# Performance work log

Hardware: AMD Instinct MI355X
Metric: run time of the kernel (lower is better)

The kernel has to match this reference:

```python
import jax, jax.numpy as jnp
import numpy as np

ROPE_DIM = 64
ROPE_THETA = 10000.0
SLIDING_WINDOW = 1024
_K_MASK = jnp.finfo(jnp.bfloat16).min


def _pos_embeddings(positions, head_dim, rope_theta):
    # positions: [B, T] -> sin, cos: [B, T, head_dim]
    fraction = jnp.arange(0, head_dim, 2, dtype=jnp.float32) / head_dim
    inv_freq = 1.0 / (rope_theta ** fraction)
    sinusoid = jnp.einsum('BT,k->BTk', positions.astype(jnp.float32), inv_freq,
                          precision=jax.lax.Precision.HIGHEST)
    sin = jnp.sin(sinusoid); cos = jnp.cos(sinusoid)
    return jnp.concatenate([sin, sin], -1), jnp.concatenate([cos, cos], -1)


def _rotate_half(x):
    x1, x2 = x[..., :x.shape[-1] // 2], x[..., x.shape[-1] // 2:]
    return jnp.concatenate([-x2, x1], -1)


def _apply_rope_partial(x, sin, cos, rope_dim):
    x_rope, x_nope = x[..., :rope_dim], x[..., rope_dim:]
    sin = sin[:, :, None, :]; cos = cos[:, :, None, :]
    x_rope = x_rope * cos + _rotate_half(x_rope) * sin
    return jnp.concatenate([x_rope, x_nope], -1).astype(x.dtype)


def setup_inputs() -> dict:
    key = jax.random.key(0)
    ks = jax.random.split(key, 6)
    B, T, D = 2, 2048, 2048
    N, K, H, Hv = 16, 4, 128, 128
    S = 2048  # cache size
    sc = 0.02
    return {
        'x': jax.random.normal(ks[0], (B, T, D), jnp.float32),
        'wq': jax.random.normal(ks[1], (D, N, H), jnp.float32) * sc,
        'wk': jax.random.normal(ks[2], (D, K, H), jnp.float32) * sc,
        'wv': jax.random.normal(ks[3], (D, K, Hv), jnp.float32) * sc,
        'wo': jax.random.normal(ks[4], (N, Hv, D), jnp.float32) * sc,
        'sink_bias': jnp.zeros((N,), jnp.float32),
        'k_cache': jnp.zeros((B, S, K, H), jnp.float32),
        'v_cache': jnp.zeros((B, S, K, Hv), jnp.float32),
        'segment_ids': jnp.ones((B, T), jnp.int32),
        'cur_ind': 0,
        'start_ind': -jnp.ones((B,), jnp.int32),
    }


def reference(x, wq, wk, wv, wo, sink_bias, k_cache, v_cache,
              segment_ids, cur_ind, start_ind):
    B, T, D = x.shape
    N, H = wq.shape[1], wq.shape[2]
    K, Hv = wk.shape[1], wv.shape[2]
    n_rep = N // K
    scaling = H ** -0.5
    cur_ind = jnp.asarray(cur_ind, jnp.int32)

    q = jnp.einsum('BTD,DNH->BTNH', x, wq)
    k = jnp.einsum('BSD,DKH->BSKH', x, wk)
    v = jnp.einsum('BSD,DKV->BSKV', x, wv)

    # left pads / positions from segment ids
    left_pads = jnp.sum(jnp.cumsum(segment_ids != 0, axis=-1) == 0, -1).astype(jnp.int32)
    start = jnp.where(start_ind < 0, left_pads, start_ind)
    pos = jax.vmap(lambda row: jnp.where(row != 0,
                                         jnp.arange(T, dtype=jnp.int32) - jnp.argmax(row).astype(jnp.int32),
                                         2 ** 30))(segment_ids) + cur_ind
    sin, cos = _pos_embeddings(pos, ROPE_DIM, ROPE_THETA)
    q = _apply_rope_partial(q, sin, cos, ROPE_DIM)
    k = _apply_rope_partial(k, sin, cos, ROPE_DIM)

    # KV cache append
    kc = jax.lax.dynamic_update_slice(k_cache, k, (0, cur_ind, 0, 0))
    vc = jax.lax.dynamic_update_slice(v_cache, v, (0, cur_ind, 0, 0))
    S = kc.shape[1]

    # GQA repeat
    kr = jnp.repeat(kc[:, :, :, None, :], n_rep, axis=3).reshape(B, S, N, H)
    vr = jnp.repeat(vc[:, :, :, None, :], n_rep, axis=3).reshape(B, S, N, Hv)

    logits = jnp.einsum('BTNH,BSNH->BTNS', q, kr) * scaling

    q_pos = cur_ind + jnp.arange(T, dtype=jnp.int32)[None, :] - start[:, None]
    ts = jnp.arange(S, dtype=jnp.int32)
    kv_seg = (ts[None, :] >= start[:, None]) & (ts[None, :] < cur_ind + T)
    k_pos = ts[None, :] - start[:, None]
    causal = k_pos[:, None, :] <= q_pos[:, :, None]
    seg_mask = kv_seg[:, None, :] == segment_ids[:, :, None]
    window = k_pos[:, None, :] >= q_pos[:, :, None] - (SLIDING_WINDOW - 1)
    final_mask = causal & seg_mask & window  # [B, T, S]
    logits = jnp.where(final_mask[:, :, None, :], logits, _K_MASK)

    # attention sink bias: extra softmax slot per head
    sink = jnp.broadcast_to(sink_bias[None, None, :, None], (B, T, N, 1))
    logits = jnp.concatenate([logits, sink], axis=-1)
    weights = jax.nn.softmax(logits.astype(jnp.float32), axis=-1).astype(logits.dtype)
    weights = weights[..., :-1]

    attn = jnp.einsum('BTNS,BSNV->BTNV', weights, vr)
    return jnp.einsum('BTNV,NVD->BTD', attn, wo)
```

## Files before the change

### kernel.cpp

```cpp
#include <hip/hip_runtime.h>
#include <hip/hip_bf16.h>
#include <stdint.h>

#define BB 2
#define TT 2048
#define DD 2048
#define NHQ 16
#define KH 4
#define HD 128
#define SS 2048
#define WINDOW 1024
#define M2FIX 12.0f
#define QSC_LOG2E 0.12751751f
#define LOG2E 1.4426950408889634f
#define NLOG2F 0.4152410118609203f

typedef __attribute__((ext_vector_type(8))) short bf16x8;
typedef __attribute__((ext_vector_type(4))) float f32x4;
typedef __attribute__((ext_vector_type(16))) float f32x16;

#define MFMA16(a, b, c) __builtin_amdgcn_mfma_f32_16x16x32_bf16(a, b, c, 0, 0, 0)
#define MFMA32(a, b, c) __builtin_amdgcn_mfma_f32_32x32x16_bf16(a, b, c, 0, 0, 0)

__device__ __forceinline__ ushort f2bf(float f) {
  uint32_t u = __float_as_uint(f);
  u += 0x7FFF + ((u >> 16) & 1);
  return (ushort)(u >> 16);
}
__device__ __forceinline__ ushort f2bf_trunc(float f) {
  return (ushort)(__float_as_uint(f) >> 16);
}
__device__ __forceinline__ float bf2f(ushort h) {
  return __uint_as_float(((uint32_t)h) << 16);
}

__device__ __forceinline__ void async_copy16(const ushort* g, ushort* l) {
  __builtin_amdgcn_global_load_lds(
      (const __attribute__((address_space(1))) uint32_t*)g,
      (__attribute__((address_space(3))) uint32_t*)l, 16, 0, 0);
}

__device__ __forceinline__ void tr_tile(const float* __restrict__ in,
                                        ushort* __restrict__ out,
                                        int C, int ldo, int cx, int cy) {
  __shared__ float tile[32][33];
  int tx = threadIdx.x & 31, ty = threadIdx.x >> 5;
  int r0 = cy * 32, c0 = cx * 32;
#pragma unroll
  for (int k = 0; k < 4; k++)
    tile[ty + k * 8][tx] = in[(size_t)(r0 + ty + k * 8) * C + c0 + tx];
  __syncthreads();
#pragma unroll
  for (int k = 0; k < 4; k++)
    out[(size_t)(c0 + ty + k * 8) * ldo + r0 + tx] = f2bf(tile[tx][ty + k * 8]);
}

__global__ void prep_fused(const float* __restrict__ x, const float* __restrict__ wq,
                           const float* __restrict__ wk, const float* __restrict__ wv,
                           const float* __restrict__ wo, const int* __restrict__ seg,
                           const int* __restrict__ start_ind, ushort* __restrict__ xb,
                           ushort* __restrict__ WcatT, ushort* __restrict__ WoT,
                           int* __restrict__ meta) {
  int bz = blockIdx.x;
  int tid = threadIdx.x;
  if (bz < 2) {
    __shared__ int red[256];
    int b = bz;
    int first = TT;
    for (int t = tid; t < TT; t += 256)
      if (seg[b * TT + t] != 0) first = min(first, t);
    red[tid] = first;
    __syncthreads();
    for (int s = 128; s > 0; s >>= 1) {
      if (tid < s) red[tid] = min(red[tid], red[tid + s]);
      __syncthreads();
    }
    if (tid == 0) {
      int fi = red[0];
      int st = start_ind[b] < 0 ? fi : start_ind[b];
      meta[b * 2 + 0] = st;
      meta[b * 2 + 1] = (fi >= TT) ? 0 : fi;
    }
    return;
  }
  bz -= 2;
  if (bz < 2048) {
#pragma unroll
    for (int p = 0; p < 4; p++) {
      int i = bz * 1024 + p * 256 + tid;
      float4 v = ((const float4*)x)[i];
      ushort4 o;
      o.x = f2bf(v.x); o.y = f2bf(v.y); o.z = f2bf(v.z); o.w = f2bf(v.w);
      ((ushort4*)xb)[i] = o;
    }
    return;
  }
  bz -= 2048;
  if (bz < 4096) { tr_tile(wq, WcatT, 2048, 2048, bz & 63, bz >> 6); return; }
  bz -= 4096;
  if (bz < 1024) { tr_tile(wk, WcatT + (size_t)2048 * 2048, 512, 2048, bz & 15, bz >> 4); return; }
  bz -= 1024;
  if (bz < 1024) { tr_tile(wv, WcatT + (size_t)2560 * 2048, 512, 2048, bz & 15, bz >> 4); return; }
  bz -= 1024;
  tr_tile(wo, WoT, 2048, 2048, bz & 63, bz >> 6);
}

__global__ void transpose_v(const ushort* __restrict__ in, ushort* __restrict__ out) {
  __shared__ ushort tile[32][33];
  int mtx = blockIdx.z;
  in  += (size_t)mtx * SS * HD;
  out += (size_t)mtx * SS * HD;
  int tx = threadIdx.x & 31, ty = threadIdx.x >> 5;
  int s0 = blockIdx.x * 32, h0 = blockIdx.y * 32;
#pragma unroll
  for (int k = 0; k < 4; k++)
    tile[ty + k * 8][tx] = in[(size_t)(s0 + ty + k * 8) * HD + h0 + tx];
  __syncthreads();
#pragma unroll
  for (int k = 0; k < 4; k++) {
    int h = h0 + ty + k * 8;
    int s = s0 + tx;
    int cit = (s & 63) >> 3;
    int sout = (s & ~63) | ((cit ^ (h & 7)) << 3) | (s & 7);
    out[(size_t)h * SS + sout] = tile[tx][ty + k * 8];
  }
}

__global__ __launch_bounds__(256) void gemm_qkv(const ushort* __restrict__ A,
                                                const ushort* __restrict__ Bt,
                                                const int* __restrict__ seg,
                                                const int* __restrict__ cur_p,
                                                const int* __restrict__ meta,
                                                ushort* __restrict__ qa,
                                                ushort* __restrict__ ka,
                                                ushort* __restrict__ va) {
  const int K = DD;
  __shared__ ushort As[128 * 64];
  __shared__ ushort Bs[128 * 64];
  __shared__ float posf_s[128];
  int tid = threadIdx.x;
  int lane = tid & 63, wave = tid >> 6;
  int wr = wave >> 1, wc = wave & 1;
  int row0 = blockIdx.y * 128, col0 = blockIdx.x * 128;
  int l31 = lane & 31, khalf = lane >> 5, lx8 = l31 & 7;
  int cur = cur_p[0];

  if (tid < 128) {
    int m = row0 + tid;
    int bb = m >> 11, t = m & 2047;
    int segv = seg[m];
    int first = meta[bb * 2 + 1];
    posf_s[tid] = (segv != 0) ? (float)(t - first + cur) : 1073741824.0f;
  }

  f32x16 acc[2][2];
#pragma unroll
  for (int i = 0; i < 2; i++)
#pragma unroll
    for (int j = 0; j < 2; j++)
#pragma unroll
      for (int e = 0; e < 16; e++) acc[i][j][e] = 0.f;

  int srow = tid >> 3, scol = tid & 7;
  int ssw = (scol ^ (srow & 7)) * 8;
  const ushort* Ag = A  + (size_t)(row0 + srow) * K + ssw;
  const ushort* Bg = Bt + (size_t)(col0 + srow) * K + ssw;
  ushort* AsD = As + tid * 8;
  ushort* BsD = Bs + tid * 8;

  for (int kc = 0; kc < K; kc += 64) {
    __syncthreads();
#pragma unroll
    for (int p = 0; p < 4; p++)
      async_copy16(Ag + kc + (size_t)(p * 32) * K, AsD + p * 2048);
#pragma unroll
    for (int p = 0; p < 4; p++)
      async_copy16(Bg + kc + (size_t)(p * 32) * K, BsD + p * 2048);
    __syncthreads();
#pragma unroll
    for (int ks = 0; ks < 4; ks++) {
      bf16x8 af[2], bfm[2];
      int ch = (ks * 2 + khalf) ^ lx8;
#pragma unroll
      for (int i = 0; i < 2; i++)
        af[i] = *(const bf16x8*)(As + (wr * 64 + i * 32 + l31) * 64 + ch * 8);
#pragma unroll
      for (int j = 0; j < 2; j++)
        bfm[j] = *(const bf16x8*)(Bs + (wc * 64 + j * 32 + l31) * 64 + ch * 8);
#pragma unroll
      for (int i = 0; i < 2; i++)
#pragma unroll
        for (int j = 0; j < 2; j++)
          acc[i][j] = MFMA32(af[i], bfm[j], acc[i][j]);
    }
  }

  int cb0 = col0 + wc * 64;
  int region = (cb0 < 2048) ? 0 : (cb0 < 2560 ? 1 : 2);
  bool ropehalf = ((cb0 & 64) == 0) && (region <= 1);
  int hbase = cb0 & 64;
  float invf = exp2f(-NLOG2F * (float)l31);

#pragma unroll
  for (int i = 0; i < 2; i++) {
#pragma unroll
    for (int reg = 0; reg < 16; reg++) {
      int rloc = wr * 64 + i * 32 + (reg & 3) + 8 * (reg >> 2) + 4 * khalf;
      int m = row0 + rloc;
      int b = m >> 11, t = m & 2047;
      float v0 = acc[i][0][reg], v1 = acc[i][1][reg];
      if (ropehalf) {
        float posf = posf_s[rloc];
        float sn, cs;
        __sincosf(posf * invf, &sn, &cs);
        float n0 = v0 * cs - v1 * sn;
        v1 = v1 * cs + v0 * sn;
        v0 = n0;
      }
      if (region == 0) {
        int head = cb0 >> 7;
        size_t base = ((size_t)(b * NHQ + head) * TT + t) * HD + hbase;
        qa[base + l31]      = f2bf(v0 * QSC_LOG2E);
        qa[base + 32 + l31] = f2bf(v1 * QSC_LOG2E);
      } else if (region == 1) {
        int head = (cb0 - 2048) >> 7;
        size_t rowbase = ((size_t)(b * KH + head) * SS + t) * HD;
        int sw = t & 7;
        int c0x = hbase + l31, c1x = hbase + 32 + l31;
        ka[rowbase + ((((c0x >> 3) ^ sw) << 3) | (c0x & 7))] = f2bf(v0);
        ka[rowbase + ((((c1x >> 3) ^ sw) << 3) | (c1x & 7))] = f2bf(v1);
      } else {
        int head = (cb0 - 2560) >> 7;
        size_t base = ((size_t)(b * KH + head) * SS + t) * HD + hbase;
        va[base + l31]      = f2bf(v0);
        va[base + 32 + l31] = f2bf(v1);
      }
    }
  }
}

template <int OUT_F32>
__global__ __launch_bounds__(256) void gemm_bt(const ushort* __restrict__ A,
                                               const ushort* __restrict__ Bt,
                                               void* __restrict__ Cout,
                                               int M, int N, int K) {
  __shared__ ushort As[128 * 64];
  __shared__ ushort Bs[128 * 64];
  int tid = threadIdx.x;
  int lane = tid & 63, wave = tid >> 6;
  int wr = wave >> 1, wc = wave & 1;
  int row0 = blockIdx.y * 128, col0 = blockIdx.x * 128;
  int l31 = lane & 31, khalf = lane >> 5, lx8 = l31 & 7;

  f32x16 acc[2][2];
#pragma unroll
  for (int i = 0; i < 2; i++)
#pragma unroll
    for (int j = 0; j < 2; j++)
#pragma unroll
      for (int e = 0; e < 16; e++) acc[i][j][e] = 0.f;

  int srow = tid >> 3, scol = tid & 7;
  int ssw = (scol ^ (srow & 7)) * 8;
  const ushort* Ag = A  + (size_t)(row0 + srow) * K + ssw;
  const ushort* Bg = Bt + (size_t)(col0 + srow) * K + ssw;
  ushort* AsD = As + tid * 8;
  ushort* BsD = Bs + tid * 8;

  for (int kc = 0; kc < K; kc += 64) {
    __syncthreads();
#pragma unroll
    for (int p = 0; p < 4; p++)
      async_copy16(Ag + kc + (size_t)(p * 32) * K, AsD + p * 2048);
#pragma unroll
    for (int p = 0; p < 4; p++)
      async_copy16(Bg + kc + (size_t)(p * 32) * K, BsD + p * 2048);
    __syncthreads();
#pragma unroll
    for (int ks = 0; ks < 4; ks++) {
      bf16x8 af[2], bfm[2];
      int ch = (ks * 2 + khalf) ^ lx8;
#pragma unroll
      for (int i = 0; i < 2; i++)
        af[i] = *(const bf16x8*)(As + (wr * 64 + i * 32 + l31) * 64 + ch * 8);
#pragma unroll
      for (int j = 0; j < 2; j++)
        bfm[j] = *(const bf16x8*)(Bs + (wc * 64 + j * 32 + l31) * 64 + ch * 8);
#pragma unroll
      for (int i = 0; i < 2; i++)
#pragma unroll
        for (int j = 0; j < 2; j++)
          acc[i][j] = MFMA32(af[i], bfm[j], acc[i][j]);
    }
  }

#pragma unroll
  for (int i = 0; i < 2; i++)
#pragma unroll
    for (int reg = 0; reg < 16; reg++) {
      int r = row0 + wr * 64 + i * 32 + (reg & 3) + 8 * (reg >> 2) + 4 * khalf;
#pragma unroll
      for (int j = 0; j < 2; j++) {
        int c = col0 + wc * 64 + j * 32 + l31;
        float v = acc[i][j][reg];
        if (OUT_F32)
          ((float*)Cout)[(size_t)r * N + c] = v;
        else
          ((ushort*)Cout)[(size_t)r * N + c] = f2bf(v);
      }
    }
}

__global__ __launch_bounds__(256) void flash_attn(
    const ushort* __restrict__ qa, const ushort* __restrict__ ka,
    const ushort* __restrict__ vat, const float* __restrict__ sink_bias,
    const int* __restrict__ seg, const int* __restrict__ cur_p,
    const int* __restrict__ meta, ushort* __restrict__ Obuf) {
  __shared__ ushort Ks[64 * 128];
  __shared__ ushort VT[128 * 64];
  __shared__ ushort Ps[4 * 16 * 64];

  int bx = blockIdx.x;
  int u = bx & 255, v = bx >> 8;
  int combo = u & 31, j5 = u >> 5;
  int b = combo >> 4, n = combo & 15;
  int qt = (v == 0) ? j5 : (v == 1) ? (15 - j5) : (v == 2) ? (16 + j5) : (31 - j5);
  int kb = n >> 2;
  int t0 = qt * 64;
  int cur = cur_p[0];
  int start = meta[b * 2];

  int tid = threadIdx.x, lane = tid & 63, w = tid >> 6;
  int lcol = lane & 15, quad = lane >> 4, lx = lcol & 7;
  int t0w = t0 + w * 16;

  const ushort* qbase = qa + (size_t)(b * NHQ + n) * TT * HD;
  const ushort* kbase = ka + (size_t)(b * KH + kb) * SS * HD;
  const ushort* vtb   = vat + (size_t)(b * KH + kb) * HD * SS;

  bf16x8 qf[4];
  {
    const ushort* qrow = qbase + (size_t)(t0w + lcol) * HD + quad * 8;
#pragma unroll
    for (int c = 0; c < 4; c++) qf[c] = *(const bf16x8*)(qrow + c * 32);
  }

  int segq[4], trow[4];
#pragma unroll
  for (int r = 0; r < 4; r++) {
    trow[r] = t0w + quad * 4 + r;
    segq[r] = seg[b * TT + trow[r]];
  }
  int seg1 = __all(segq[0] == 1 && segq[1] == 1 && segq[2] == 1 && segq[3] == 1);

  f32x4 oacc[8], lacc;
#pragma unroll
  for (int ob = 0; ob < 8; ob++) { f32x4 z = {0.f, 0.f, 0.f, 0.f}; oacc[ob] = z; }
  { f32x4 z = {0.f, 0.f, 0.f, 0.f}; lacc = z; }

  bf16x8 ones;
#pragma unroll
  for (int e = 0; e < 8; e++) ones[e] = (short)0x3F80;

  ushort* KsD = Ks + tid * 8;
  ushort* VTD = VT + tid * 8;
  const ushort* KgT = kbase + tid * 8;
  const ushort* VgT = vtb + (size_t)(tid >> 3) * SS + (tid & 7) * 8;

  int lo = cur + t0 - (WINDOW - 1); if (lo < 0) lo = 0;
  int hi = cur + t0 + 63;           if (hi > SS - 1) hi = SS - 1;
  int ktlo = lo >> 6, kthi = hi >> 6;

  ushort* PsW = Ps + w * 1024;

  for (int kt = ktlo; kt <= kthi; kt++) {
    int ks0 = kt * 64;
    __syncthreads();
#pragma unroll
    for (int p = 0; p < 4; p++)
      async_copy16(KgT + (size_t)ks0 * 128 + p * 2048, KsD + p * 2048);
#pragma unroll
    for (int p = 0; p < 4; p++)
      async_copy16(VgT + ks0 + (size_t)p * 32 * SS, VTD + p * 2048);
    __syncthreads();

    bool active = (ks0 <= cur + t0w + 15) && (ks0 + 63 >= cur + t0w - (WINDOW - 1));
    if (active) {
      f32x4 sacc[4];
#pragma unroll
      for (int cb = 0; cb < 4; cb++) { f32x4 z = {0.f, 0.f, 0.f, 0.f}; sacc[cb] = z; }
#pragma unroll
      for (int c = 0; c < 4; c++) {
#pragma unroll
        for (int cb = 0; cb < 4; cb++) {
          bf16x8 kf = *(const bf16x8*)(Ks + (cb * 16 + lcol) * 128 +
                                       (((c * 4 + quad) ^ lx)) * 8);
          sacc[cb] = MFMA16(qf[c], kf, sacc[cb]);
        }
      }

      bool fast = seg1 && (ks0 >= start) && (ks0 + 63 <= cur + t0w) &&
                  (ks0 >= cur + t0w + 15 - (WINDOW - 1));
      if (fast) {
#pragma unroll
        for (int r = 0; r < 4; r++) {
          int row = quad * 4 + r;
#pragma unroll
          for (int cb = 0; cb < 4; cb++) {
            float p = exp2f(sacc[cb][r] - M2FIX);
            PsW[row * 64 + (((cb * 2 + (lcol >> 3)) ^ (row & 7)) * 8) + lx] = f2bf_trunc(p);
          }
        }
      } else {
        int sidx[4], kvseg[4];
#pragma unroll
        for (int cb = 0; cb < 4; cb++) {
          sidx[cb] = ks0 + cb * 16 + lcol;
          kvseg[cb] = (sidx[cb] >= start && sidx[cb] < cur + TT) ? 1 : 0;
        }
#pragma unroll
        for (int r = 0; r < 4; r++) {
          int row = quad * 4 + r;
          int qp = (segq[r] != 0) ? (cur + trow[r]) : (1 << 29);
#pragma unroll
          for (int cb = 0; cb < 4; cb++) {
            bool ok = (sidx[cb] <= qp) && (sidx[cb] >= qp - (WINDOW - 1)) &&
                      (kvseg[cb] == segq[r]);
            float p = ok ? exp2f(sacc[cb][r] - M2FIX) : 0.f;
            PsW[row * 64 + (((cb * 2 + (lcol >> 3)) ^ (row & 7)) * 8) + lx] = f2bf_trunc(p);
          }
        }
      }

#pragma unroll
      for (int c2 = 0; c2 < 2; c2++) {
        bf16x8 pf = *(const bf16x8*)(PsW + lcol * 64 + (((c2 * 4 + quad) ^ lx)) * 8);
#pragma unroll
        for (int ob = 0; ob < 8; ob++) {
          bf16x8 vf = *(const bf16x8*)(VT + (ob * 16 + lcol) * 64 +
                                       (((c2 * 4 + quad) ^ lx)) * 8);
          oacc[ob] = MFMA16(pf, vf, oacc[ob]);
        }
        lacc = MFMA16(pf, ones, lacc);
      }
    }
  }

  float sb = sink_bias[n];
#pragma unroll
  for (int r = 0; r < 4; r++) {
    float l = lacc[r] + exp2f(sb * LOG2E - M2FIX);
    float inv = 1.f / l;
    int t = trow[r];
    size_t base = ((size_t)(b * TT + t)) * (NHQ * HD) + n * HD;
#pragma unroll
    for (int ob = 0; ob < 8; ob++)
      Obuf[base + ob * 16 + lcol] = f2bf(oacc[ob][r] * inv);
  }
}

extern "C" void kernel_launch(void* const* d_in, const int* in_sizes, int n_in,
                              void* d_out, int out_size, void* d_ws, size_t ws_size,
                              hipStream_t stream) {
  const float* x  = (const float*)d_in[0];
  const float* wq = (const float*)d_in[1];
  const float* wk = (const float*)d_in[2];
  const float* wv = (const float*)d_in[3];
  const float* wo = (const float*)d_in[4];
  const float* sink = (const float*)d_in[5];
  const int* seg = (const int*)d_in[8];
  const int* cur = (const int*)d_in[9];
  const int* start_ind = (const int*)d_in[10];

  char* ws = (char*)d_ws;
  ushort* xb    = (ushort*)(ws + 0);
  ushort* WcatT = (ushort*)(ws + 16777216);
  ushort* WoT   = (ushort*)(ws + 29360128);
  ushort* qa    = (ushort*)(ws + 37748736);
  ushort* ka    = (ushort*)(ws + 54525952);
  ushort* va    = (ushort*)(ws + 58720256);
  ushort* vat   = (ushort*)(ws + 62914560);
  ushort* Obuf  = (ushort*)(ws + 67108864);
  int*    meta  = (int*)(ws + 83886080);

  prep_fused<<<12290, 256, 0, stream>>>(x, wq, wk, wv, wo, seg, start_ind,
                                        xb, WcatT, WoT, meta);
  gemm_qkv<<<dim3(24, 32), 256, 0, stream>>>(xb, WcatT, seg, cur, meta, qa, ka, va);
  transpose_v<<<dim3(64, 4, 8), 256, 0, stream>>>(va, vat);
  flash_attn<<<1024, 256, 0, stream>>>(qa, ka, vat, sink, seg, cur, meta, Obuf);
  gemm_bt<1><<<dim3(16, 32), 256, 0, stream>>>(Obuf, WoT, d_out, 4096, 2048, 2048);
}
```

Before: 296.6 us.

## Enlarge transpose and attention tiles, add extra LDS swizzle bits in GEMMs

The weight transpose-and-convert now works on 64x64 tiles instead of 32x32, which cuts the prep grid from 12290 to 4610 blocks. Flash attention now runs 512-thread blocks over 128-query tiles with 8 waves, so each K/V tile loaded into LDS is shared by twice as many query rows, and the query-tile order is interleaved for load balance. Both GEMMs XOR extra row bits into the LDS swizzle to reduce bank conflicts on the 32-row MFMA fragment reads. Risks are lower occupancy from larger blocks and LDS, and coarser work units in attention.

Measured after the change: 313.7 us. 1.06x slower.

```diff
diff --git a/kernel.cpp b/kernel.cpp
--- a/kernel.cpp
+++ b/kernel.cpp
@@ -40,19 +40,23 @@
       (__attribute__((address_space(3))) uint32_t*)l, 16, 0, 0);
 }
 
-__device__ __forceinline__ void tr_tile(const float* __restrict__ in,
-                                        ushort* __restrict__ out,
-                                        int C, int ldo, int cx, int cy) {
-  __shared__ float tile[32][33];
-  int tx = threadIdx.x & 31, ty = threadIdx.x >> 5;
-  int r0 = cy * 32, c0 = cx * 32;
-#pragma unroll
-  for (int k = 0; k < 4; k++)
-    tile[ty + k * 8][tx] = in[(size_t)(r0 + ty + k * 8) * C + c0 + tx];
+__device__ __forceinline__ void tr_tile64(const float* __restrict__ in,
+                                          ushort* __restrict__ out,
+                                          int C, int ldo, int cx, int cy) {
+  __shared__ float tile[64][65];
+  int tx = threadIdx.x & 63, ty = threadIdx.x >> 6;
+  int r0 = cy * 64, c0 = cx * 64;
+#pragma unroll
+  for (int k = 0; k < 16; k++) {
+    int row = k * 4 + ty;
+    tile[row][tx] = in[(size_t)(r0 + row) * C + c0 + tx];
+  }
   __syncthreads();
 #pragma unroll
-  for (int k = 0; k < 4; k++)
-    out[(size_t)(c0 + ty + k * 8) * ldo + r0 + tx] = f2bf(tile[tx][ty + k * 8]);
+  for (int k = 0; k < 16; k++) {
+    int c = k * 4 + ty;
+    out[(size_t)(c0 + c) * ldo + r0 + tx] = f2bf(tile[tx][c]);
+  }
 }
 
 __global__ void prep_fused(const float* __restrict__ x, const float* __restrict__ wq,
@@ -96,13 +100,13 @@
     return;
   }
   bz -= 2048;
-  if (bz < 4096) { tr_tile(wq, WcatT, 2048, 2048, bz & 63, bz >> 6); return; }
-  bz -= 4096;
-  if (bz < 1024) { tr_tile(wk, WcatT + (size_t)2048 * 2048, 512, 2048, bz & 15, bz >> 4); return; }
+  if (bz < 1024) { tr_tile64(wq, WcatT, 2048, 2048, bz & 31, bz >> 5); return; }
   bz -= 1024;
-  if (bz < 1024) { tr_tile(wv, WcatT + (size_t)2560 * 2048, 512, 2048, bz & 15, bz >> 4); return; }
-  bz -= 1024;
-  tr_tile(wo, WoT, 2048, 2048, bz & 63, bz >> 6);
+  if (bz < 256)  { tr_tile64(wk, WcatT + (size_t)2048 * 2048, 512, 2048, bz & 7, bz >> 3); return; }
+  bz -= 256;
+  if (bz < 256)  { tr_tile64(wv, WcatT + (size_t)2560 * 2048, 512, 2048, bz & 7, bz >> 3); return; }
+  bz -= 256;
+  tr_tile64(wo, WoT, 2048, 2048, bz & 31, bz >> 5);
 }
 
 __global__ void transpose_v(const ushort* __restrict__ in, ushort* __restrict__ out) {
@@ -143,6 +147,7 @@
   int wr = wave >> 1, wc = wave & 1;
   int row0 = blockIdx.y * 128, col0 = blockIdx.x * 128;
   int l31 = lane & 31, khalf = lane >> 5, lx8 = l31 & 7;
+  int rsw = lx8 ^ ((l31 >> 3) & 3);
   int cur = cur_p[0];
 
   if (tid < 128) {
@@ -162,7 +167,7 @@
       for (int e = 0; e < 16; e++) acc[i][j][e] = 0.f;
 
   int srow = tid >> 3, scol = tid & 7;
-  int ssw = (scol ^ (srow & 7)) * 8;
+  int ssw = (scol ^ (srow & 7) ^ ((srow >> 3) & 3)) * 8;
   const ushort* Ag = A  + (size_t)(row0 + srow) * K + ssw;
   const ushort* Bg = Bt + (size_t)(col0 + srow) * K + ssw;
   ushort* AsD = As + tid * 8;
@@ -180,7 +185,7 @@
 #pragma unroll
     for (int ks = 0; ks < 4; ks++) {
       bf16x8 af[2], bfm[2];
-      int ch = (ks * 2 + khalf) ^ lx8;
+      int ch = (ks * 2 + khalf) ^ rsw;
 #pragma unroll
       for (int i = 0; i < 2; i++)
         af[i] = *(const bf16x8*)(As + (wr * 64 + i * 32 + l31) * 64 + ch * 8);
@@ -251,6 +256,7 @@
   int wr = wave >> 1, wc = wave & 1;
   int row0 = blockIdx.y * 128, col0 = blockIdx.x * 128;
   int l31 = lane & 31, khalf = lane >> 5, lx8 = l31 & 7;
+  int rsw = lx8 ^ ((l31 >> 3) & 3);
 
   f32x16 acc[2][2];
 #pragma unroll
@@ -261,7 +267,7 @@
       for (int e = 0; e < 16; e++) acc[i][j][e] = 0.f;
 
   int srow = tid >> 3, scol = tid & 7;
-  int ssw = (scol ^ (srow & 7)) * 8;
+  int ssw = (scol ^ (srow & 7) ^ ((srow >> 3) & 3)) * 8;
   const ushort* Ag = A  + (size_t)(row0 + srow) * K + ssw;
   const ushort* Bg = Bt + (size_t)(col0 + srow) * K + ssw;
   ushort* AsD = As + tid * 8;
@@ -279,7 +285,7 @@
 #pragma unroll
     for (int ks = 0; ks < 4; ks++) {
       bf16x8 af[2], bfm[2];
-      int ch = (ks * 2 + khalf) ^ lx8;
+      int ch = (ks * 2 + khalf) ^ rsw;
 #pragma unroll
       for (int i = 0; i < 2; i++)
         af[i] = *(const bf16x8*)(As + (wr * 64 + i * 32 + l31) * 64 + ch * 8);
@@ -311,22 +317,22 @@
     }
 }
 
-__global__ __launch_bounds__(256) void flash_attn(
+__global__ __launch_bounds__(512) void flash_attn(
     const ushort* __restrict__ qa, const ushort* __restrict__ ka,
     const ushort* __restrict__ vat, const float* __restrict__ sink_bias,
     const int* __restrict__ seg, const int* __restrict__ cur_p,
     const int* __restrict__ meta, ushort* __restrict__ Obuf) {
   __shared__ ushort Ks[64 * 128];
   __shared__ ushort VT[128 * 64];
-  __shared__ ushort Ps[4 * 16 * 64];
+  __shared__ ushort Ps[8 * 16 * 64];
 
   int bx = blockIdx.x;
-  int u = bx & 255, v = bx >> 8;
-  int combo = u & 31, j5 = u >> 5;
-  int b = combo >> 4, n = combo & 15;
-  int qt = (v == 0) ? j5 : (v == 1) ? (15 - j5) : (v == 2) ? (16 + j5) : (31 - j5);
+  int b = bx & 1;
+  int n = (bx >> 1) & 15;
+  int g = bx >> 5;
+  int qp = (g & 1) ? (15 - (g >> 1)) : (g >> 1);
   int kb = n >> 2;
-  int t0 = qt * 64;
+  int t0 = qp * 128;
   int cur = cur_p[0];
   int start = meta[b * 2];
 
@@ -368,7 +374,7 @@
   const ushort* VgT = vtb + (size_t)(tid >> 3) * SS + (tid & 7) * 8;
 
   int lo = cur + t0 - (WINDOW - 1); if (lo < 0) lo = 0;
-  int hi = cur + t0 + 63;           if (hi > SS - 1) hi = SS - 1;
+  int hi = cur + t0 + 127;          if (hi > SS - 1) hi = SS - 1;
   int ktlo = lo >> 6, kthi = hi >> 6;
 
   ushort* PsW = Ps + w * 1024;
@@ -377,11 +383,11 @@
     int ks0 = kt * 64;
     __syncthreads();
 #pragma unroll
-    for (int p = 0; p < 4; p++)
-      async_copy16(KgT + (size_t)ks0 * 128 + p * 2048, KsD + p * 2048);
-#pragma unroll
-    for (int p = 0; p < 4; p++)
-      async_copy16(VgT + ks0 + (size_t)p * 32 * SS, VTD + p * 2048);
+    for (int p = 0; p < 2; p++)
+      async_copy16(KgT + (size_t)ks0 * 128 + p * 4096, KsD + p * 4096);
+#pragma unroll
+    for (int p = 0; p < 2; p++)
+      async_copy16(VgT + ks0 + (size_t)(p * 64) * SS, VTD + p * 4096);
     __syncthreads();
 
     bool active = (ks0 <= cur + t0w + 15) && (ks0 + 63 >= cur + t0w - (WINDOW - 1));
@@ -421,10 +427,10 @@
 #pragma unroll
         for (int r = 0; r < 4; r++) {
           int row = quad * 4 + r;
-          int qp = (segq[r] != 0) ? (cur + trow[r]) : (1 << 29);
+          int qp2 = (segq[r] != 0) ? (cur + trow[r]) : (1 << 29);
 #pragma unroll
           for (int cb = 0; cb < 4; cb++) {
-            bool ok = (sidx[cb] <= qp) && (sidx[cb] >= qp - (WINDOW - 1)) &&
+            bool ok = (sidx[cb] <= qp2) && (sidx[cb] >= qp2 - (WINDOW - 1)) &&
                       (kvseg[cb] == segq[r]);
             float p = ok ? exp2f(sacc[cb][r] - M2FIX) : 0.f;
             PsW[row * 64 + (((cb * 2 + (lcol >> 3)) ^ (row & 7)) * 8) + lx] = f2bf_trunc(p);
@@ -483,10 +489,10 @@
   ushort* Obuf  = (ushort*)(ws + 67108864);
   int*    meta  = (int*)(ws + 83886080);
 
-  prep_fused<<<12290, 256, 0, stream>>>(x, wq, wk, wv, wo, seg, start_ind,
-                                        xb, WcatT, WoT, meta);
+  prep_fused<<<4610, 256, 0, stream>>>(x, wq, wk, wv, wo, seg, start_ind,
+                                       xb, WcatT, WoT, meta);
   gemm_qkv<<<dim3(24, 32), 256, 0, stream>>>(xb, WcatT, seg, cur, meta, qa, ka, va);
   transpose_v<<<dim3(64, 4, 8), 256, 0, stream>>>(va, vat);
-  flash_attn<<<1024, 256, 0, stream>>>(qa, ka, vat, sink, seg, cur, meta, Obuf);
+  flash_attn<<<512, 512, 0, stream>>>(qa, ka, vat, sink, seg, cur, meta, Obuf);
   gemm_bt<1><<<dim3(16, 32), 256, 0, stream>>>(Obuf, WoT, d_out, 4096, 2048, 2048);
 }
```
